# Optimization experiments

Hardware: AMD Instinct MI355X
Metric: run time of the kernel (lower is better)

Reference implementation:

```python
import jax, jax.numpy as jnp
import numpy as np

B, S, NQ, D, K = 8, 43, 13, 608, 4  # batch, seq, query nodes, d_model, top-k


def setup_inputs() -> dict:
    key = jax.random.key(0)
    k1, k2, k3 = jax.random.split(key, 3)
    x = jax.random.normal(k1, (B, S, D), dtype=jnp.float32)        # encoder output
    scores = jax.random.normal(k2, (B, S, S), dtype=jnp.float32)   # last-layer attn scores
    W_ff = jax.random.normal(k3, (2 * D, 4), dtype=jnp.float32) * 0.02
    b_ff = jnp.zeros((4,), dtype=jnp.float32)
    return {"x": x, "scores": scores, "W_ff": W_ff, "b_ff": b_ff}


def reference(x, scores, W_ff, b_ff):
    x13 = x[:, :NQ, :]                                   # [B,13,608]
    imp = scores.reshape(-1, S, S)[:, :NQ, :NQ]          # [B,13,13]
    _, idx = jax.lax.top_k(imp, K)                       # [B,13,4] int32, distinct per row
    # gather top-k neighbor features: gathered[b,i,j] = x13[b, idx[b,i,j]]
    gathered = jax.vmap(lambda xb, ib: xb[ib])(x13, idx)            # [B,13,4,608]
    self_feat = jnp.broadcast_to(x13[:, :, None, :], gathered.shape)
    pair = jnp.concatenate([self_feat, gathered], axis=-1)         # [B,13,4,1216]
    vals = pair @ W_ff + b_ff                                       # [B,13,4,4]
    # out initialized to one-hot [1,0,0,0] everywhere, then scatter ff outputs
    base = jnp.zeros((B, NQ, NQ, 4), dtype=jnp.float32).at[..., 0].set(1.0)
    bb = jnp.arange(B)[:, None, None]
    ii = jnp.arange(NQ)[None, :, None]
    out = base.at[bb, ii, idx].set(vals)                            # [B,13,13,4]
    return out
```

## Files before the change

### kernel.cpp

```cpp
#include <hip/hip_runtime.h>

#define NB 8
#define SS 43
#define NQ 13
#define DD 608
#define KK 4
#define NF4 (DD / 4)

__global__ __launch_bounds__(256) void imp_enc_kernel(
    const float* __restrict__ x, const float* __restrict__ scores,
    const float* __restrict__ Wff, const float* __restrict__ bff,
    float* __restrict__ out)
{
    const int bi   = blockIdx.x;
    const int b    = bi / NQ;
    const int i    = bi % NQ;
    const int k    = threadIdx.x >> 6;
    const int lane = threadIdx.x & 63;

    const float4* W4  = (const float4*)Wff;
    const float4* xs4 = (const float4*)(x + ((size_t)b * SS + i) * DD);

    const float* srow = scores + ((size_t)b * SS + i) * SS;
    float sv[NQ];
    #pragma unroll
    for (int m = 0; m < NQ; ++m) sv[m] = srow[m];
    float myv = (lane < NQ) ? srow[lane] : -INFINITY;
    float4 bias = *(const float4*)bff;

    int rank = 0;
    #pragma unroll
    for (int m = 0; m < NQ; ++m)
        rank += (sv[m] > myv || (sv[m] == myv && m < lane)) ? 1 : 0;

    int idx[KK];
    #pragma unroll
    for (int kk = 0; kk < KK; ++kk) {
        unsigned long long msk = __ballot(lane < NQ && rank == kk);
        idx[kk] = (int)__ffsll(msk) - 1;
    }

    const float4* xg4 = (const float4*)(x + ((size_t)b * SS + idx[k]) * DD);
    float4 gv0, gv1, gv2;
    {
        const int f0 = lane, f1 = lane + 64, f2 = lane + 128;
        gv0 = xg4[f0];
        gv1 = xg4[f1];
        gv2 = (f2 < NF4) ? xg4[f2] : make_float4(0.f, 0.f, 0.f, 0.f);
    }

    float acc[4] = {0.f, 0.f, 0.f, 0.f};
    #pragma unroll
    for (int it = 0; it < 3; ++it) {
        const int f = lane + it * 64;
        if (f < NF4) {
            float4 xv = xs4[f];
            const float xe[4] = {xv.x, xv.y, xv.z, xv.w};
            #pragma unroll
            for (int u = 0; u < 4; ++u) {
                float4 wt = W4[f * 4 + u];
                acc[0] += xe[u] * wt.x;
                acc[1] += xe[u] * wt.y;
                acc[2] += xe[u] * wt.z;
                acc[3] += xe[u] * wt.w;
            }
        }
    }

    #pragma unroll
    for (int it = 0; it < 3; ++it) {
        const int f = lane + it * 64;
        if (f < NF4) {
            float4 gvv = (it == 0) ? gv0 : (it == 1) ? gv1 : gv2;
            const float ge[4] = {gvv.x, gvv.y, gvv.z, gvv.w};
            #pragma unroll
            for (int u = 0; u < 4; ++u) {
                float4 wb = W4[DD + f * 4 + u];
                acc[0] += ge[u] * wb.x;
                acc[1] += ge[u] * wb.y;
                acc[2] += ge[u] * wb.z;
                acc[3] += ge[u] * wb.w;
            }
        }
    }

    #pragma unroll
    for (int off = 32; off > 0; off >>= 1) {
        #pragma unroll
        for (int c = 0; c < 4; ++c) acc[c] += __shfl_xor(acc[c], off, 64);
    }

    if (lane < NQ * 4) {
        const int j = lane >> 2;
        const int c = lane & 3;
        const float vA = (c & 2) ? ((c & 1) ? acc[3] : acc[2])
                                 : ((c & 1) ? acc[1] : acc[0]);
        const float bc = (c & 2) ? ((c & 1) ? bias.w : bias.z)
                                 : ((c & 1) ? bias.y : bias.x);
        const bool sel = (j == idx[0]) | (j == idx[1]) | (j == idx[2]) | (j == idx[3]);
        float* orow = out + (size_t)bi * (NQ * 4);
        if (j == idx[k]) {
            orow[lane] = vA + bc;
        } else if (k == 0 && !sel) {
            orow[lane] = (c == 0) ? 1.0f : 0.0f;
        }
    }
}

extern "C" void kernel_launch(void* const* d_in, const int* in_sizes, int n_in,
                              void* d_out, int out_size, void* d_ws, size_t ws_size,
                              hipStream_t stream) {
    const float* x      = (const float*)d_in[0];
    const float* scores = (const float*)d_in[1];
    const float* Wff    = (const float*)d_in[2];
    const float* bff    = (const float*)d_in[3];
    float* out = (float*)d_out;

    imp_enc_kernel<<<NB * NQ, 256, 0, stream>>>(x, scores, Wff, bff, out);
}
```

Before: 11.43 us.

## Prefetch batch rows cooperatively and defer top-k until after self-half dot

Each block now loads all 13 query rows of its batch into cache with a cooperative prefetch loop, so the later dependent gather of neighbor rows hits cache. The top-k rank computation is moved after the self-feature dot product and uses wave shuffles instead of 13 per-lane scalar loads of the score row. This takes the score-load-to-gather dependency chain off the critical path. In exchange every block issues redundant prefetch loads of roughly 31 KB, which adds memory traffic across the 104 blocks.

```diff
diff --git a/kernel.cpp b/kernel.cpp
--- a/kernel.cpp
+++ b/kernel.cpp
@@ -6,6 +6,7 @@
 #define DD 608
 #define KK 4
 #define NF4 (DD / 4)
+#define PF4 (NQ * NF4)
 
 __global__ __launch_bounds__(256) void imp_enc_kernel(
     const float* __restrict__ x, const float* __restrict__ scores,
@@ -15,39 +16,26 @@
     const int bi   = blockIdx.x;
     const int b    = bi / NQ;
     const int i    = bi % NQ;
-    const int k    = threadIdx.x >> 6;
-    const int lane = threadIdx.x & 63;
+    const int tid  = threadIdx.x;
+    const int k    = tid >> 6;
+    const int lane = tid & 63;
 
     const float4* W4  = (const float4*)Wff;
-    const float4* xs4 = (const float4*)(x + ((size_t)b * SS + i) * DD);
+    const float4* xb4 = (const float4*)(x + (size_t)b * SS * DD);
+    const float4* xs4 = xb4 + (size_t)i * NF4;
 
-    const float* srow = scores + ((size_t)b * SS + i) * SS;
-    float sv[NQ];
     #pragma unroll
-    for (int m = 0; m < NQ; ++m) sv[m] = srow[m];
-    float myv = (lane < NQ) ? srow[lane] : -INFINITY;
-    float4 bias = *(const float4*)bff;
-
-    int rank = 0;
-    #pragma unroll
-    for (int m = 0; m < NQ; ++m)
-        rank += (sv[m] > myv || (sv[m] == myv && m < lane)) ? 1 : 0;
-
-    int idx[KK];
-    #pragma unroll
-    for (int kk = 0; kk < KK; ++kk) {
-        unsigned long long msk = __ballot(lane < NQ && rank == kk);
-        idx[kk] = (int)__ffsll(msk) - 1;
+    for (int r = 0; r < 8; ++r) {
+        const int q = tid + r * 256;
+        if (q < PF4) {
+            float4 pf = xb4[q];
+            asm volatile("" :: "v"(pf.x), "v"(pf.y), "v"(pf.z), "v"(pf.w));
+        }
     }
 
-    const float4* xg4 = (const float4*)(x + ((size_t)b * SS + idx[k]) * DD);
-    float4 gv0, gv1, gv2;
-    {
-        const int f0 = lane, f1 = lane + 64, f2 = lane + 128;
-        gv0 = xg4[f0];
-        gv1 = xg4[f1];
-        gv2 = (f2 < NF4) ? xg4[f2] : make_float4(0.f, 0.f, 0.f, 0.f);
-    }
+    float4 bias = *(const float4*)bff;
+    const float* srow = scores + ((size_t)b * SS + i) * SS;
+    float myv = (lane < NQ) ? srow[lane] : -INFINITY;
 
     float acc[4] = {0.f, 0.f, 0.f, 0.f};
     #pragma unroll
@@ -67,12 +55,26 @@
         }
     }
 
+    int rank = 0;
+    #pragma unroll
+    for (int m = 0; m < NQ; ++m) {
+        float vm = __shfl(myv, m, 64);
+        if (vm > myv || (vm == myv && m < lane)) ++rank;
+    }
+    int idx[KK];
+    #pragma unroll
+    for (int kk = 0; kk < KK; ++kk) {
+        unsigned long long msk = __ballot(lane < NQ && rank == kk);
+        idx[kk] = (int)__ffsll(msk) - 1;
+    }
+
+    const float4* xg4 = xb4 + (size_t)idx[k] * NF4;
     #pragma unroll
     for (int it = 0; it < 3; ++it) {
         const int f = lane + it * 64;
         if (f < NF4) {
-            float4 gvv = (it == 0) ? gv0 : (it == 1) ? gv1 : gv2;
-            const float ge[4] = {gvv.x, gvv.y, gvv.z, gvv.w};
+            float4 gv = xg4[f];
+            const float ge[4] = {gv.x, gv.y, gv.z, gv.w};
             #pragma unroll
             for (int u = 0; u < 4; ++u) {
                 float4 wb = W4[DD + f * 4 + u];
```

After: 9.932 us. 1.15x faster.
